# Kernel optimization log

Hardware: AMD Instinct MI355X
Metric: run time of the kernel (lower is better)

Reference implementation:

```python
import jax, jax.numpy as jnp
import numpy as np

B, S, D = 1, 2048, 2048
NH, NKV, HD = 32, 8, 64
EPS = 1e-5
SCALE = float(HD) ** 0.5


def _rope(x, cos, sin):
    # x: [b, h, s, hd]; cos/sin: [s, hd//2]; interleaved-pair rotary (executorch style)
    xr = x[..., 0::2]
    xi = x[..., 1::2]
    c = cos[None, None, :, :]
    s = sin[None, None, :, :]
    out_r = xr * c - xi * s
    out_i = xr * s + xi * c
    return jnp.stack([out_r, out_i], axis=-1).reshape(x.shape)


def _rmsnorm(x, w):
    var = jnp.mean(x * x, axis=-1, keepdims=True)
    return x * jax.lax.rsqrt(var + EPS) * w


def setup_inputs() -> dict:
    key = jax.random.key(0)
    ks = jax.random.split(key, 6)
    hidden_states = jax.random.normal(ks[0], (B, S, D), dtype=jnp.float32)
    # standard Llama rope tables, theta=10000
    inv_freq = 1.0 / (10000.0 ** (np.arange(0, HD, 2, dtype=np.float32) / HD))
    t = np.arange(S, dtype=np.float32)
    ang = np.outer(t, inv_freq)  # [S, HD//2]
    freqs_cos = jnp.asarray(np.cos(ang), dtype=jnp.float32)
    freqs_sin = jnp.asarray(np.sin(ang), dtype=jnp.float32)
    # additive causal mask [1,1,S,S]
    causal = jnp.tril(jnp.ones((S, S), dtype=bool))
    atten_mask = jnp.where(causal, 0.0, -1e9).astype(jnp.float32)[None, None]
    sd = 1.0 / np.sqrt(D)
    wq = jax.random.normal(ks[1], (NH * HD, D), dtype=jnp.float32) * sd
    wk = jax.random.normal(ks[2], (NKV * HD, D), dtype=jnp.float32) * sd
    wv = jax.random.normal(ks[3], (NKV * HD, D), dtype=jnp.float32) * sd
    wo = jax.random.normal(ks[4], (D, NH * HD), dtype=jnp.float32) * sd
    q_norm_w = jnp.ones((HD,), dtype=jnp.float32)
    k_norm_w = jnp.ones((HD,), dtype=jnp.float32)
    return dict(hidden_states=hidden_states, freqs_cos=freqs_cos, freqs_sin=freqs_sin,
                atten_mask=atten_mask, wq=wq, wk=wk, wv=wv, wo=wo,
                q_norm_w=q_norm_w, k_norm_w=k_norm_w)


def reference(hidden_states, freqs_cos, freqs_sin, atten_mask, wq, wk, wv, wo, q_norm_w, k_norm_w):
    b, s, _ = hidden_states.shape
    n_rep = NH // NKV
    # fused QKV projections (Linear: x @ W.T)
    q = (hidden_states @ wq.T).reshape(b, s, NH, HD).transpose(0, 2, 1, 3)   # [b,nh,s,hd]
    k = (hidden_states @ wk.T).reshape(b, s, NKV, HD).transpose(0, 2, 1, 3)  # [b,nkv,s,hd]
    v = (hidden_states @ wv.T).reshape(b, s, NKV, HD).transpose(0, 2, 1, 3)
    # RoPE, then QK RMSNorm (qk_norm_before_rope=False)
    q = _rope(q, freqs_cos, freqs_sin)
    k = _rope(k, freqs_cos, freqs_sin)
    q = _rmsnorm(q, q_norm_w)
    k = _rmsnorm(k, k_norm_w)
    # no KV cache (prefill): kh = k^T, vh = v, then GQA repeat
    kh = jnp.repeat(k, n_rep, axis=1)  # [b,nh,s,hd]
    vh = jnp.repeat(v, n_rep, axis=1)
    attn = jnp.einsum('bhqd,bhkd->bhqk', q, kh) / SCALE
    attn = jax.nn.softmax(attn + atten_mask, axis=-1)
    y = jnp.einsum('bhqk,bhkd->bhqd', attn, vh)
    y = y.transpose(0, 2, 1, 3).reshape(b, s, NH * HD)
    y = y @ wo.T
    # module returns (y, [kh], [vh]); kh stored transposed (b,nh,hd,s)
    return (y, kh.transpose(0, 1, 3, 2), vh)
```

## Files before the change

kernel.cpp:

```cpp
#include <hip/hip_runtime.h>
#include <cstdint>
#include <cstddef>

#define S_   2048
#define D_   2048
#define NH_  32
#define NKV_ 8
#define HD_  64

using bf16x8 = __attribute__((ext_vector_type(8))) __bf16;
using f32x4  = __attribute__((ext_vector_type(4))) float;

#define AS_GLOBAL(p) (const __attribute__((address_space(1))) void*)(p)
#define AS_LDS(p)    (__attribute__((address_space(3))) void*)(p)

__device__ __forceinline__ float b2f(uint u) {
  union { uint u; float f; } c; c.u = u << 16; return c.f;
}

__global__ __launch_bounds__(256) void cvt_all(
    const float* __restrict__ hs, const float* __restrict__ wq,
    const float* __restrict__ wk, const float* __restrict__ wv,
    const float* __restrict__ wo,
    __bf16* __restrict__ hs_bf, __bf16* __restrict__ wq_bf,
    __bf16* __restrict__ wk_bf, __bf16* __restrict__ wv_bf,
    __bf16* __restrict__ wo_bf) {
  int i = blockIdx.x * 256 + threadIdx.x;
  const float* src; __bf16* dst; int base;
  if (i < 1048576)      { src = hs; dst = hs_bf; base = 0; }
  else if (i < 2097152) { src = wq; dst = wq_bf; base = 1048576; }
  else if (i < 2359296) { src = wk; dst = wk_bf; base = 2097152; }
  else if (i < 2621440) { src = wv; dst = wv_bf; base = 2359296; }
  else                  { src = wo; dst = wo_bf; base = 2621440; }
  i -= base;
  const float4 v = reinterpret_cast<const float4*>(src)[i];
  __bf16 t[4] = {(__bf16)v.x, (__bf16)v.y, (__bf16)v.z, (__bf16)v.w};
  reinterpret_cast<uint2*>(dst)[i] = *reinterpret_cast<uint2*>(t);
}

__device__ __forceinline__ void gemm_compute_step(
    const char* ldsA, const char* ldsB, f32x4 (&acc)[4][4],
    int l15, int lg, int wm, int wn) {
  bf16x8 af[4][2], bfr[4][2];
#pragma unroll
  for (int f = 0; f < 4; ++f) {
    const int arow = wm*64 + f*16 + l15;
    const int brow = wn*64 + f*16 + l15;
#pragma unroll
    for (int ks = 0; ks < 2; ++ks) {
      af[f][ks] = *reinterpret_cast<const bf16x8*>(
          ldsA + arow*128 + (((ks*4 + lg) ^ (arow & 7)) << 4));
      bfr[f][ks] = *reinterpret_cast<const bf16x8*>(
          ldsB + brow*128 + (((ks*4 + lg) ^ (brow & 7)) << 4));
    }
  }
#pragma unroll
  for (int mf = 0; mf < 4; ++mf)
#pragma unroll
    for (int nf = 0; nf < 4; ++nf) {
      acc[mf][nf] = __builtin_amdgcn_mfma_f32_16x16x32_bf16(
          af[mf][0], bfr[nf][0], acc[mf][nf], 0, 0, 0);
      acc[mf][nf] = __builtin_amdgcn_mfma_f32_16x16x32_bf16(
          af[mf][1], bfr[nf][1], acc[mf][nf], 0, 0, 0);
    }
}

template <int MODE>
__device__ __forceinline__ void gemm_tile_128_bf(
    char (*lds)[32768],
    const __bf16* __restrict__ A, const __bf16* __restrict__ B,
    __bf16* __restrict__ C, int K, int N, int m0, int n0,
    const float* __restrict__ cosT, const float* __restrict__ sinT,
    const float* __restrict__ nw) {
  const int tid = threadIdx.x;
  const int l = tid & 63;
  const int w = tid >> 6;
  const int l15 = l & 15, lg = l >> 4;
  const int wm = w >> 1, wn = w & 1;

  f32x4 acc[4][4] = {};

  const int srow   = tid >> 3;
  const int schunk = (tid & 7) ^ (srow & 7);
  const __bf16* gA = A + (size_t)(m0 + srow) * K + schunk * 8;
  const __bf16* gB = B + (size_t)(n0 + srow) * K + schunk * 8;
  const int ldst = tid * 16;
  const int nt = K >> 6;

#pragma unroll
  for (int i = 0; i < 4; ++i) {
    __builtin_amdgcn_global_load_lds(AS_GLOBAL(gA + (size_t)i*32*K),
                                     AS_LDS(&lds[0][i*4096 + ldst]), 16, 0, 0);
    __builtin_amdgcn_global_load_lds(AS_GLOBAL(gB + (size_t)i*32*K),
                                     AS_LDS(&lds[0][16384 + i*4096 + ldst]), 16, 0, 0);
  }
  __syncthreads();

  int cur = 0;
  for (int t = 0; t < nt; ++t) {
    if (t + 1 < nt) {
      const int k0 = (t + 1) * 64;
      char* dA = &lds[cur ^ 1][0];
      char* dB = &lds[cur ^ 1][16384];
#pragma unroll
      for (int i = 0; i < 4; ++i) {
        __builtin_amdgcn_global_load_lds(AS_GLOBAL(gA + (size_t)i*32*K + k0),
                                         AS_LDS(dA + i*4096 + ldst), 16, 0, 0);
        __builtin_amdgcn_global_load_lds(AS_GLOBAL(gB + (size_t)i*32*K + k0),
                                         AS_LDS(dB + i*4096 + ldst), 16, 0, 0);
      }
    }
    gemm_compute_step(&lds[cur][0], &lds[cur][16384], acc, l15, lg, wm, wn);
    __syncthreads();
    cur ^= 1;
  }

  if constexpr (MODE == 0) {
#pragma unroll
    for (int mf = 0; mf < 4; ++mf)
#pragma unroll
      for (int nf = 0; nf < 4; ++nf)
#pragma unroll
        for (int r = 0; r < 4; ++r)
          C[(size_t)(m0 + wm*64 + mf*16 + lg*4 + r) * N + n0 + wn*64 + nf*16 + l15]
              = (__bf16)acc[mf][nf][r];
  } else {
    const float fin = (MODE == 1) ? 0.180336880111120426f : 1.0f;
    float wv_[4];
#pragma unroll
    for (int nf = 0; nf < 4; ++nf) wv_[nf] = nw[nf*16 + l15];
    const int odd = l15 & 1;
#pragma unroll
    for (int mf = 0; mf < 4; ++mf) {
#pragma unroll
      for (int r = 0; r < 4; ++r) {
        const int row = m0 + wm*64 + mf*16 + lg*4 + r;
        float ro[4];
        float ssq = 0.f;
#pragma unroll
        for (int nf = 0; nf < 4; ++nf) {
          const float v = acc[mf][nf][r];
          const float p = __shfl_xor(v, 1);
          const int d2 = (nf*16 + l15) >> 1;
          const float c  = cosT[row*32 + d2];
          const float sn = sinT[row*32 + d2];
          ro[nf] = odd ? fmaf(p, sn, v*c) : fmaf(v, c, -p*sn);
          ssq = fmaf(ro[nf], ro[nf], ssq);
        }
        ssq += __shfl_xor(ssq, 1);
        ssq += __shfl_xor(ssq, 2);
        ssq += __shfl_xor(ssq, 4);
        ssq += __shfl_xor(ssq, 8);
        const float rinv = rsqrtf(ssq * (1.0f/64.0f) + 1e-5f);
#pragma unroll
        for (int nf = 0; nf < 4; ++nf)
          C[(size_t)row * N + n0 + wn*64 + nf*16 + l15]
              = (__bf16)(ro[nf] * rinv * wv_[nf] * fin);
      }
    }
  }
}

__device__ __forceinline__ void gemm_tile_128_d2(
    const __bf16* __restrict__ A, const __bf16* __restrict__ B,
    float* __restrict__ C, int K, int N, int m0, int n0) {
  __shared__ __align__(16) char lds[3][32768];
  const int tid = threadIdx.x;
  const int l = tid & 63;
  const int w = tid >> 6;
  const int l15 = l & 15, lg = l >> 4;
  const int wm = w >> 1, wn = w & 1;

  f32x4 acc[4][4] = {};

  const int srow   = tid >> 3;
  const int schunk = (tid & 7) ^ (srow & 7);
  const __bf16* gA = A + (size_t)(m0 + srow) * K + schunk * 8;
  const __bf16* gB = B + (size_t)(n0 + srow) * K + schunk * 8;
  const int ldst = tid * 16;
  const int nt = K >> 6;

#pragma unroll
  for (int i = 0; i < 4; ++i) {
    __builtin_amdgcn_global_load_lds(AS_GLOBAL(gA + (size_t)i*32*K),
                                     AS_LDS(&lds[0][i*4096 + ldst]), 16, 0, 0);
    __builtin_amdgcn_global_load_lds(AS_GLOBAL(gB + (size_t)i*32*K),
                                     AS_LDS(&lds[0][16384 + i*4096 + ldst]), 16, 0, 0);
  }
#pragma unroll
  for (int i = 0; i < 4; ++i) {
    __builtin_amdgcn_global_load_lds(AS_GLOBAL(gA + (size_t)i*32*K + 64),
                                     AS_LDS(&lds[1][i*4096 + ldst]), 16, 0, 0);
    __builtin_amdgcn_global_load_lds(AS_GLOBAL(gB + (size_t)i*32*K + 64),
                                     AS_LDS(&lds[1][16384 + i*4096 + ldst]), 16, 0, 0);
  }

  char* p0 = &lds[0][0];
  char* p1 = &lds[1][0];
  char* p2 = &lds[2][0];

  for (int t = 0; t < nt; ++t) {
    if (t + 1 < nt) asm volatile("s_waitcnt vmcnt(8)" ::: "memory");
    else            asm volatile("s_waitcnt vmcnt(0)" ::: "memory");
    __builtin_amdgcn_s_barrier();

    if (t + 2 < nt) {
      const int k0 = (t + 2) * 64;
#pragma unroll
      for (int i = 0; i < 4; ++i) {
        __builtin_amdgcn_global_load_lds(AS_GLOBAL(gA + (size_t)i*32*K + k0),
                                         AS_LDS(p2 + i*4096 + ldst), 16, 0, 0);
        __builtin_amdgcn_global_load_lds(AS_GLOBAL(gB + (size_t)i*32*K + k0),
                                         AS_LDS(p2 + 16384 + i*4096 + ldst), 16, 0, 0);
      }
    }

    gemm_compute_step(p0, p0 + 16384, acc, l15, lg, wm, wn);

    char* tmp = p0; p0 = p1; p1 = p2; p2 = tmp;
  }

#pragma unroll
  for (int mf = 0; mf < 4; ++mf)
#pragma unroll
    for (int nf = 0; nf < 4; ++nf)
#pragma unroll
      for (int r = 0; r < 4; ++r)
        C[(size_t)(m0 + wm*64 + mf*16 + lg*4 + r) * N + n0 + wn*64 + nf*16 + l15]
            = acc[mf][nf][r];
}

__global__ __launch_bounds__(256) void gemm_qkv(
    const __bf16* __restrict__ hs,
    const __bf16* __restrict__ wq, const __bf16* __restrict__ wk,
    const __bf16* __restrict__ wv,
    __bf16* __restrict__ qbf, __bf16* __restrict__ kbf, __bf16* __restrict__ vp,
    const float* __restrict__ fcos, const float* __restrict__ fsin,
    const float* __restrict__ qw, const float* __restrict__ kw) {
  __shared__ __align__(16) char lds[2][32768];
  const int bx = blockIdx.x;
  const int m0 = blockIdx.y * 128;
  if (bx < 16) {
    gemm_tile_128_bf<1>(lds, hs, wq, qbf, 2048, 2048, m0, bx*128, fcos, fsin, qw);
  } else if (bx < 20) {
    gemm_tile_128_bf<2>(lds, hs, wk, kbf, 2048, 512, m0, (bx-16)*128, fcos, fsin, kw);
  } else {
    gemm_tile_128_bf<0>(lds, hs, wv, vp, 2048, 512, m0, (bx-20)*128,
                        nullptr, nullptr, nullptr);
  }
}

__global__ __launch_bounds__(256) void gemm_wo(
    const __bf16* __restrict__ ypre, const __bf16* __restrict__ wo,
    float* __restrict__ y) {
  gemm_tile_128_d2(ypre, wo, y, 2048, 2048, blockIdx.y * 128, blockIdx.x * 128);
}

__global__ __launch_bounds__(256) void transpose_kv(
    const __bf16* __restrict__ kpost, float* __restrict__ khT,
    const __bf16* __restrict__ vp, float* __restrict__ vh,
    __bf16* __restrict__ vtbf) {
  __shared__ float tl[64][68];
  const int kvh = blockIdx.y;
  const int t = threadIdx.x;
  if (blockIdx.x < 32) {
    const int s0 = blockIdx.x * 64;
    {
      const int d0 = (t & 15) * 4;
      const int sl = t >> 4;
#pragma unroll
      for (int rep = 0; rep < 4; ++rep) {
        const int srow = sl + rep*16;
        const uint2 v = *reinterpret_cast<const uint2*>(
            &kpost[(size_t)(s0 + srow)*(NKV_*HD_) + kvh*HD_ + d0]);
        tl[d0+0][srow] = b2f(v.x & 0xffff);
        tl[d0+1][srow] = b2f(v.x >> 16);
        tl[d0+2][srow] = b2f(v.y & 0xffff);
        tl[d0+3][srow] = b2f(v.y >> 16);
      }
    }
    __syncthreads();
    {
      const int d  = t >> 2;
      const int s4 = (t & 3) * 16;
#pragma unroll
      for (int c = 0; c < 4; ++c) {
        float4 v;
        v.x = tl[d][s4+c*4+0]; v.y = tl[d][s4+c*4+1];
        v.z = tl[d][s4+c*4+2]; v.w = tl[d][s4+c*4+3];
#pragma unroll
        for (int r = 0; r < 4; ++r) {
          *reinterpret_cast<float4*>(
              &khT[((size_t)(kvh*4 + r)*HD_ + d)*S_ + s0 + s4 + c*4]) = v;
        }
      }
    }
  } else {
    const int s0 = (blockIdx.x - 32) * 64;
    const int srow = t >> 2, dc = (t & 3) * 16;
    const __bf16* src = &vp[(size_t)(s0 + srow)*(NKV_*HD_) + kvh*HD_ + dc];
    const uint4 a = reinterpret_cast<const uint4*>(src)[0];
    const uint4 b = reinterpret_cast<const uint4*>(src)[1];
    float f[16];
    f[0]=b2f(a.x&0xffff); f[1]=b2f(a.x>>16); f[2]=b2f(a.y&0xffff); f[3]=b2f(a.y>>16);
    f[4]=b2f(a.z&0xffff); f[5]=b2f(a.z>>16); f[6]=b2f(a.w&0xffff); f[7]=b2f(a.w>>16);
    f[8]=b2f(b.x&0xffff); f[9]=b2f(b.x>>16); f[10]=b2f(b.y&0xffff); f[11]=b2f(b.y>>16);
    f[12]=b2f(b.z&0xffff); f[13]=b2f(b.z>>16); f[14]=b2f(b.w&0xffff); f[15]=b2f(b.w>>16);
#pragma unroll
    for (int i = 0; i < 16; ++i) tl[srow][dc + i] = f[i];
#pragma unroll
    for (int r = 0; r < 4; ++r) {
      float* dst = &vh[((size_t)(kvh*4 + r)*S_ + s0 + srow)*HD_ + dc];
#pragma unroll
      for (int cc = 0; cc < 4; ++cc) {
        float4 v4 = {f[cc*4+0], f[cc*4+1], f[cc*4+2], f[cc*4+3]};
        reinterpret_cast<float4*>(dst)[cc] = v4;
      }
    }
    __syncthreads();
    const int dr = t >> 2, sc = (t & 3) * 16;
    __bf16 vals[16];
#pragma unroll
    for (int i = 0; i < 16; ++i) vals[i] = (__bf16)tl[sc + i][dr];
    uint4* dst = reinterpret_cast<uint4*>(&vtbf[((size_t)(kvh*64 + dr))*S_ + s0 + sc]);
    dst[0] = reinterpret_cast<uint4*>(vals)[0];
    dst[1] = reinterpret_cast<uint4*>(vals)[1];
  }
}

__device__ __forceinline__ uint pack2bf(float a, float b) {
  __bf16 x = (__bf16)a, y = (__bf16)b;
  const uint ux = (uint)*reinterpret_cast<ushort*>(&x);
  const uint uy = (uint)*reinterpret_cast<ushort*>(&y);
  return ux | (uy << 16);
}

__device__ __forceinline__ void qk_tile_T(
    const char* kldh, bf16x8 qf0, bf16x8 qf1, f32x4 (&s_)[4],
    int l15, int lg) {
  __builtin_amdgcn_s_setprio(1);
#pragma unroll
  for (int nb = 0; nb < 4; ++nb) {
    const int row = nb*16 + l15;
    const int bc  = lg*16;
    const bf16x8 kb0 = *reinterpret_cast<const bf16x8*>(
        kldh + row*128 + ((bc)      ^ ((row & 7) << 4)));
    const bf16x8 kb1 = *reinterpret_cast<const bf16x8*>(
        kldh + row*128 + ((bc + 64) ^ ((row & 7) << 4)));
    f32x4 t = f32x4{0.f, 0.f, 0.f, 0.f};
    t = __builtin_amdgcn_mfma_f32_16x16x32_bf16(kb0, qf0, t, 0, 0, 0);
    t = __builtin_amdgcn_mfma_f32_16x16x32_bf16(kb1, qf1, t, 0, 0, 0);
    s_[nb] = t;
  }
  __builtin_amdgcn_s_setprio(0);
}

__device__ __forceinline__ void softmax_pv_T(
    f32x4 (&s_)[4], float& m_, float& l_, f32x4 (&o_)[4],
    char* pldw, const char* vbase, int l15, int lg) {
  float mx = fmaxf(fmaxf(s_[0][0], s_[0][1]), fmaxf(s_[0][2], s_[0][3]));
#pragma unroll
  for (int nb = 1; nb < 4; ++nb) {
    mx = fmaxf(mx, fmaxf(fmaxf(s_[nb][0], s_[nb][1]),
                         fmaxf(s_[nb][2], s_[nb][3])));
  }
  mx = fmaxf(mx, __shfl_xor(mx, 16));
  mx = fmaxf(mx, __shfl_xor(mx, 32));

  if (!__all(mx <= m_ + 8.f)) {
    const float mnew = fmaxf(m_, mx);
    const float scl = exp2f(m_ - mnew);
    m_ = mnew;
    l_ *= scl;
#pragma unroll
    for (int nb = 0; nb < 4; ++nb) {
      o_[nb][0] *= scl; o_[nb][1] *= scl; o_[nb][2] *= scl; o_[nb][3] *= scl;
    }
  }

  const int swz = (l15 & 7) << 4;
  float ls = 0.f;
#pragma unroll
  for (int nb = 0; nb < 4; ++nb) {
    float p0 = exp2f(s_[nb][0] - m_);
    float p1 = exp2f(s_[nb][1] - m_);
    float p2 = exp2f(s_[nb][2] - m_);
    float p3 = exp2f(s_[nb][3] - m_);
    ls += (p0 + p1) + (p2 + p3);
    *reinterpret_cast<uint*>(pldw + ((l15*128 + nb*32 + lg*8)     ^ swz)) = pack2bf(p0, p1);
    *reinterpret_cast<uint*>(pldw + ((l15*128 + nb*32 + lg*8 + 4) ^ swz)) = pack2bf(p2, p3);
  }
  ls += __shfl_xor(ls, 16);
  ls += __shfl_xor(ls, 32);
  l_ += ls;

  const bf16x8 pb0 = *reinterpret_cast<const bf16x8*>(
      pldw + ((l15*128 + lg*16)      ^ swz));
  const bf16x8 pb1 = *reinterpret_cast<const bf16x8*>(
      pldw + ((l15*128 + lg*16 + 64) ^ swz));

  __builtin_amdgcn_s_setprio(1);
#pragma unroll
  for (int nb = 0; nb < 4; ++nb) {
    const int row = nb*16 + l15;
    const int bc  = lg*16;
    const bf16x8 v0 = *reinterpret_cast<const bf16x8*>(
        vbase + row*128 + ((bc)      ^ ((row & 7) << 4)));
    const bf16x8 v1 = *reinterpret_cast<const bf16x8*>(
        vbase + row*128 + ((bc + 64) ^ ((row & 7) << 4)));
    f32x4 t = o_[nb];
    t = __builtin_amdgcn_mfma_f32_16x16x32_bf16(v0, pb0, t, 0, 0, 0);
    t = __builtin_amdgcn_mfma_f32_16x16x32_bf16(v1, pb1, t, 0, 0, 0);
    o_[nb] = t;
  }
  __builtin_amdgcn_s_setprio(0);
}

__device__ __forceinline__ void mask_diag_T(f32x4 (&s_)[4], int l15, int lg, int wg) {
  const int qrow = wg*16 + l15;
#pragma unroll
  for (int nb = 0; nb < 4; ++nb)
#pragma unroll
    for (int r = 0; r < 4; ++r)
      if (nb*16 + lg*4 + r > qrow) s_[nb][r] = -1e30f;
}

__global__ __launch_bounds__(512, 4) void flash_attn_mfma(
    const __bf16* __restrict__ qbf, const __bf16* __restrict__ kbf,
    const __bf16* __restrict__ vtbf, __bf16* __restrict__ ypre) {
  __shared__ __align__(16) char smem[49152];

  const int h   = blockIdx.y;
  const int pi  = blockIdx.x;
  const int qbA = pi, qbB = 31 - pi;
  const int SS  = (qbB >> 1) + 1;
  const int kvh = h >> 2;
  const int tid = threadIdx.x;
  const int l   = tid & 63;
  const int w   = tid >> 6;
  const int g   = tid >> 8;
  const int wg  = w & 3;
  const int l15 = l & 15;
  const int lg  = l >> 4;

  char* kldg = smem + g*8192;
  char* vtlg = smem + 16384 + g*8192;
  char* pldw = smem + 32768 + w*2048;

  const int ts = tid & 255;
  const int j  = ts >> 2;
  const int c0 = (ts & 3) * 16;
  const int b0 = (j*128 + c0*2)      ^ ((j & 7) << 4);
  const int b1 = (j*128 + c0*2 + 16) ^ ((j & 7) << 4);
  const __bf16* ksrc = kbf  + (size_t)(g*64 + j)*(NKV_*HD_) + kvh*HD_ + c0;
  const __bf16* vsrc = vtbf + (size_t)(kvh*64 + j)*S_ + g*64 + c0;

  bf16x8 qfA0, qfA1, qfB0, qfB1;
  {
    const __bf16* qa = qbf + (size_t)(qbA*64 + wg*16 + l15)*D_ + h*HD_ + lg*8;
    qfA0 = *reinterpret_cast<const bf16x8*>(qa);
    qfA1 = *reinterpret_cast<const bf16x8*>(qa + 32);
    const __bf16* qb = qbf + (size_t)(qbB*64 + wg*16 + l15)*D_ + h*HD_ + lg*8;
    qfB0 = *reinterpret_cast<const bf16x8*>(qb);
    qfB1 = *reinterpret_cast<const bf16x8*>(qb + 32);
  }

  f32x4 oA[4], oB[4];
#pragma unroll
  for (int nb = 0; nb < 4; ++nb) {
    oA[nb] = f32x4{0.f, 0.f, 0.f, 0.f};
    oB[nb] = f32x4{0.f, 0.f, 0.f, 0.f};
  }
  float mA = -1e30f, lA = 0.f, mB = -1e30f, lB = 0.f;

  uint4 kr0 = reinterpret_cast<const uint4*>(ksrc)[0];
  uint4 kr1 = reinterpret_cast<const uint4*>(ksrc + 8)[0];
  uint4 vr0 = reinterpret_cast<const uint4*>(vsrc)[0];
  uint4 vr1 = reinterpret_cast<const uint4*>(vsrc + 8)[0];

  for (int st = 0; st < SS; ++st) {
    __syncthreads();
    *reinterpret_cast<uint4*>(kldg + b0) = kr0;
    *reinterpret_cast<uint4*>(kldg + b1) = kr1;
    *reinterpret_cast<uint4*>(vtlg + b0) = vr0;
    *reinterpret_cast<uint4*>(vtlg + b1) = vr1;
    __syncthreads();

    if (st + 1 < SS) {
      const __bf16* kn = ksrc + (size_t)(st + 1)*128*(NKV_*HD_);
      const __bf16* vn = vsrc + (size_t)(st + 1)*128;
      kr0 = reinterpret_cast<const uint4*>(kn)[0];
      kr1 = reinterpret_cast<const uint4*>(kn + 8)[0];
      vr0 = reinterpret_cast<const uint4*>(vn)[0];
      vr1 = reinterpret_cast<const uint4*>(vn + 8)[0];
    }

    const int kt = 2*st + g;
    if (kt <= qbB) {
      f32x4 s_[4];
      qk_tile_T(kldg, qfB0, qfB1, s_, l15, lg);
      if (kt == qbB) mask_diag_T(s_, l15, lg, wg);
      softmax_pv_T(s_, mB, lB, oB, pldw, vtlg, l15, lg);
    }
    if (kt <= qbA) {
      f32x4 s_[4];
      qk_tile_T(kldg, qfA0, qfA1, s_, l15, lg);
      if (kt == qbA) mask_diag_T(s_, l15, lg, wg);
      softmax_pv_T(s_, mA, lA, oA, pldw, vtlg, l15, lg);
    }
  }

  float* ox = reinterpret_cast<float*>(smem);
  float* ml = reinterpret_cast<float*>(smem + 20480);
  float* po = ox + (wg*64 + l)*17;
  float* pm = ml + (wg*64 + l)*9;

  __syncthreads();
  if (g == 1) {
#pragma unroll
    for (int nb = 0; nb < 4; ++nb)
#pragma unroll
      for (int r = 0; r < 4; ++r) po[nb*4 + r] = oB[nb][r];
    pm[0] = mB; pm[1] = lB;
  }
  __syncthreads();
  if (g == 0) {
    const float m1 = pm[0], l1 = pm[1];
    const float m = fmaxf(mB, m1);
    const float s0 = exp2f(mB - m), s1 = exp2f(m1 - m);
    lB = lB*s0 + l1*s1;
#pragma unroll
    for (int nb = 0; nb < 4; ++nb)
#pragma unroll
      for (int r = 0; r < 4; ++r)
        oB[nb][r] = oB[nb][r]*s0 + po[nb*4 + r]*s1;
  }
  __syncthreads();
  if (g == 1) {
#pragma unroll
    for (int nb = 0; nb < 4; ++nb)
#pragma unroll
      for (int r = 0; r < 4; ++r) po[nb*4 + r] = oA[nb][r];
    pm[0] = mA; pm[1] = lA;
  }
  __syncthreads();
  if (g == 0) {
    const float m1 = pm[0], l1 = pm[1];
    const float m = fmaxf(mA, m1);
    const float s0 = exp2f(mA - m), s1 = exp2f(m1 - m);
    lA = lA*s0 + l1*s1;
#pragma unroll
    for (int nb = 0; nb < 4; ++nb)
#pragma unroll
      for (int r = 0; r < 4; ++r)
        oA[nb][r] = oA[nb][r]*s0 + po[nb*4 + r]*s1;

    const float rlA = 1.0f / lA, rlB = 1.0f / lB;
    const size_t rowA = (size_t)(qbA*64 + wg*16 + l15)*D_ + h*HD_;
    const size_t rowB = (size_t)(qbB*64 + wg*16 + l15)*D_ + h*HD_;
#pragma unroll
    for (int nb = 0; nb < 4; ++nb) {
      uint2 pa, pb;
      pa.x = pack2bf(oA[nb][0]*rlA, oA[nb][1]*rlA);
      pa.y = pack2bf(oA[nb][2]*rlA, oA[nb][3]*rlA);
      pb.x = pack2bf(oB[nb][0]*rlB, oB[nb][1]*rlB);
      pb.y = pack2bf(oB[nb][2]*rlB, oB[nb][3]*rlB);
      *reinterpret_cast<uint2*>(&ypre[rowA + nb*16 + lg*4]) = pa;
      *reinterpret_cast<uint2*>(&ypre[rowB + nb*16 + lg*4]) = pb;
    }
  }
}

extern "C" void kernel_launch(void* const* d_in, const int* in_sizes, int n_in,
                              void* d_out, int out_size, void* d_ws, size_t ws_size,
                              hipStream_t stream) {
  (void)in_sizes; (void)n_in; (void)out_size;
  const float* hs   = (const float*)d_in[0];
  const float* fcos = (const float*)d_in[1];
  const float* fsin = (const float*)d_in[2];
  const float* wq = (const float*)d_in[4];
  const float* wk = (const float*)d_in[5];
  const float* wv = (const float*)d_in[6];
  const float* wo = (const float*)d_in[7];
  const float* qw = (const float*)d_in[8];
  const float* kw = (const float*)d_in[9];

  float* out = (float*)d_out;
  float* y   = out;
  float* khT = out + 4194304;
  float* vh  = out + 8388608;

  __bf16* qbf   = (__bf16*)y;
  __bf16* kbf   = (__bf16*)((char*)y + 8*1024*1024);
  __bf16* vtbf  = (__bf16*)((char*)y + 10*1024*1024);
  __bf16* hs_bf = (__bf16*)khT;
  __bf16* wq_bf = (__bf16*)((char*)khT + 8*1024*1024);
  __bf16* wk_bf = (__bf16*)vh;
  __bf16* wv_bf = (__bf16*)((char*)vh + 2*1024*1024);

  const size_t need = (size_t)40 * 1024 * 1024;
  if (ws_size < need) return;
  char* ws = (char*)d_ws;
  __bf16* vp_bf   = (__bf16*)(ws);
  __bf16* ypre_bf = (__bf16*)(ws + 2*1024*1024);
  __bf16* wo_bf   = (__bf16*)(ws + 10*1024*1024);

  cvt_all<<<14336, 256, 0, stream>>>(hs, wq, wk, wv, wo,
                                     hs_bf, wq_bf, wk_bf, wv_bf, wo_bf);

  gemm_qkv<<<dim3(24, 16), 256, 0, stream>>>(hs_bf, wq_bf, wk_bf, wv_bf,
                                             qbf, kbf, vp_bf,
                                             fcos, fsin, qw, kw);

  transpose_kv<<<dim3(64, 8), 256, 0, stream>>>(kbf, khT, vp_bf, vh, vtbf);

  flash_attn_mfma<<<dim3(16, 32), 512, 0, stream>>>(qbf, kbf, vtbf, ypre_bf);

  gemm_wo<<<dim3(16, 16), 256, 0, stream>>>(ypre_bf, wo_bf, y);
}
```

Measured before the change: 139.6 us.

## Triple-buffer QKV GEMM and widen Q tiles to 128x256

Reworks the fused QKV projection GEMM into a three-stage LDS pipeline that uses explicit vmcnt waits and a single barrier per k-step, instead of double buffering with two syncs. Q-projection blocks now compute 128x256 tiles (8 N-fragments per wave), so the A tile is reused across more columns and the grid shrinks from 24 to 16 columns. The RoPE+RMSNorm epilogue is regrouped per 64-wide head. The cost is 144KB of LDS per block, which limits occupancy to one block per CU, plus more accumulator registers for the wide tiles.

```diff
diff --git a/kernel.cpp b/kernel.cpp
--- a/kernel.cpp
+++ b/kernel.cpp
@@ -65,9 +65,9 @@
     }
 }
 
-template <int MODE>
-__device__ __forceinline__ void gemm_tile_128_bf(
-    char (*lds)[32768],
+template <int MODE, int NW>
+__device__ __forceinline__ void gemm_tile_d2x(
+    char (*lds)[49152],
     const __bf16* __restrict__ A, const __bf16* __restrict__ B,
     __bf16* __restrict__ C, int K, int N, int m0, int n0,
     const float* __restrict__ cosT, const float* __restrict__ sinT,
@@ -78,7 +78,7 @@
   const int l15 = l & 15, lg = l >> 4;
   const int wm = w >> 1, wn = w & 1;
 
-  f32x4 acc[4][4] = {};
+  f32x4 acc[4][NW] = {};
 
   const int srow   = tid >> 3;
   const int schunk = (tid & 7) ^ (srow & 7);
@@ -87,75 +87,109 @@
   const int ldst = tid * 16;
   const int nt = K >> 6;
 
-#pragma unroll
-  for (int i = 0; i < 4; ++i) {
-    __builtin_amdgcn_global_load_lds(AS_GLOBAL(gA + (size_t)i*32*K),
-                                     AS_LDS(&lds[0][i*4096 + ldst]), 16, 0, 0);
-    __builtin_amdgcn_global_load_lds(AS_GLOBAL(gB + (size_t)i*32*K),
-                                     AS_LDS(&lds[0][16384 + i*4096 + ldst]), 16, 0, 0);
-  }
-  __syncthreads();
-
-  int cur = 0;
+  auto stage = [&](char* buf, int k0) {
+#pragma unroll
+    for (int i = 0; i < 4; ++i)
+      __builtin_amdgcn_global_load_lds(AS_GLOBAL(gA + (size_t)i*32*K + k0),
+                                       AS_LDS(buf + i*4096 + ldst), 16, 0, 0);
+#pragma unroll
+    for (int i = 0; i < NW; ++i)
+      __builtin_amdgcn_global_load_lds(AS_GLOBAL(gB + (size_t)i*32*K + k0),
+                                       AS_LDS(buf + 16384 + i*4096 + ldst), 16, 0, 0);
+  };
+
+  stage(&lds[0][0], 0);
+  stage(&lds[1][0], 64);
+
+  char* p0 = &lds[0][0];
+  char* p1 = &lds[1][0];
+  char* p2 = &lds[2][0];
+
   for (int t = 0; t < nt; ++t) {
     if (t + 1 < nt) {
-      const int k0 = (t + 1) * 64;
-      char* dA = &lds[cur ^ 1][0];
-      char* dB = &lds[cur ^ 1][16384];
-#pragma unroll
-      for (int i = 0; i < 4; ++i) {
-        __builtin_amdgcn_global_load_lds(AS_GLOBAL(gA + (size_t)i*32*K + k0),
-                                         AS_LDS(dA + i*4096 + ldst), 16, 0, 0);
-        __builtin_amdgcn_global_load_lds(AS_GLOBAL(gB + (size_t)i*32*K + k0),
-                                         AS_LDS(dB + i*4096 + ldst), 16, 0, 0);
+      if constexpr (NW == 8) asm volatile("s_waitcnt vmcnt(12)" ::: "memory");
+      else                   asm volatile("s_waitcnt vmcnt(8)"  ::: "memory");
+    } else {
+      asm volatile("s_waitcnt vmcnt(0)" ::: "memory");
+    }
+    __builtin_amdgcn_s_barrier();
+
+    if (t + 2 < nt) stage(p2, (t + 2) * 64);
+
+    {
+      bf16x8 af[4][2];
+#pragma unroll
+      for (int f = 0; f < 4; ++f) {
+        const int arow = wm*64 + f*16 + l15;
+#pragma unroll
+        for (int ks = 0; ks < 2; ++ks)
+          af[f][ks] = *reinterpret_cast<const bf16x8*>(
+              p0 + arow*128 + (((ks*4 + lg) ^ (arow & 7)) << 4));
       }
-    }
-    gemm_compute_step(&lds[cur][0], &lds[cur][16384], acc, l15, lg, wm, wn);
-    __syncthreads();
-    cur ^= 1;
+#pragma unroll
+      for (int nf = 0; nf < NW; ++nf) {
+        const int brow = wn*(NW*16) + nf*16 + l15;
+        const bf16x8 b0 = *reinterpret_cast<const bf16x8*>(
+            p0 + 16384 + brow*128 + (((lg)     ^ (brow & 7)) << 4));
+        const bf16x8 b1 = *reinterpret_cast<const bf16x8*>(
+            p0 + 16384 + brow*128 + (((4 + lg) ^ (brow & 7)) << 4));
+#pragma unroll
+        for (int mf = 0; mf < 4; ++mf) {
+          acc[mf][nf] = __builtin_amdgcn_mfma_f32_16x16x32_bf16(
+              af[mf][0], b0, acc[mf][nf], 0, 0, 0);
+          acc[mf][nf] = __builtin_amdgcn_mfma_f32_16x16x32_bf16(
+              af[mf][1], b1, acc[mf][nf], 0, 0, 0);
+        }
+      }
+    }
+
+    char* tmp = p0; p0 = p1; p1 = p2; p2 = tmp;
   }
 
   if constexpr (MODE == 0) {
 #pragma unroll
     for (int mf = 0; mf < 4; ++mf)
 #pragma unroll
-      for (int nf = 0; nf < 4; ++nf)
+      for (int nf = 0; nf < NW; ++nf)
 #pragma unroll
         for (int r = 0; r < 4; ++r)
-          C[(size_t)(m0 + wm*64 + mf*16 + lg*4 + r) * N + n0 + wn*64 + nf*16 + l15]
-              = (__bf16)acc[mf][nf][r];
+          C[(size_t)(m0 + wm*64 + mf*16 + lg*4 + r) * N
+            + n0 + wn*(NW*16) + nf*16 + l15] = (__bf16)acc[mf][nf][r];
   } else {
     const float fin = (MODE == 1) ? 0.180336880111120426f : 1.0f;
-    float wv_[4];
-#pragma unroll
-    for (int nf = 0; nf < 4; ++nf) wv_[nf] = nw[nf*16 + l15];
+    float wv4[4];
+#pragma unroll
+    for (int j = 0; j < 4; ++j) wv4[j] = nw[j*16 + l15];
     const int odd = l15 & 1;
 #pragma unroll
     for (int mf = 0; mf < 4; ++mf) {
 #pragma unroll
       for (int r = 0; r < 4; ++r) {
         const int row = m0 + wm*64 + mf*16 + lg*4 + r;
-        float ro[4];
-        float ssq = 0.f;
-#pragma unroll
-        for (int nf = 0; nf < 4; ++nf) {
-          const float v = acc[mf][nf][r];
-          const float p = __shfl_xor(v, 1);
-          const int d2 = (nf*16 + l15) >> 1;
-          const float c  = cosT[row*32 + d2];
-          const float sn = sinT[row*32 + d2];
-          ro[nf] = odd ? fmaf(p, sn, v*c) : fmaf(v, c, -p*sn);
-          ssq = fmaf(ro[nf], ro[nf], ssq);
+#pragma unroll
+        for (int grp = 0; grp < NW/4; ++grp) {
+          float ro[4];
+          float ssq = 0.f;
+#pragma unroll
+          for (int j = 0; j < 4; ++j) {
+            const float v = acc[mf][grp*4 + j][r];
+            const float p = __shfl_xor(v, 1);
+            const int d2 = (j*16 + l15) >> 1;
+            const float c  = cosT[row*32 + d2];
+            const float sn = sinT[row*32 + d2];
+            ro[j] = odd ? fmaf(p, sn, v*c) : fmaf(v, c, -p*sn);
+            ssq = fmaf(ro[j], ro[j], ssq);
+          }
+          ssq += __shfl_xor(ssq, 1);
+          ssq += __shfl_xor(ssq, 2);
+          ssq += __shfl_xor(ssq, 4);
+          ssq += __shfl_xor(ssq, 8);
+          const float rinv = rsqrtf(ssq * (1.0f/64.0f) + 1e-5f);
+#pragma unroll
+          for (int j = 0; j < 4; ++j)
+            C[(size_t)row * N + n0 + wn*(NW*16) + (grp*4 + j)*16 + l15]
+                = (__bf16)(ro[j] * rinv * wv4[j] * fin);
         }
-        ssq += __shfl_xor(ssq, 1);
-        ssq += __shfl_xor(ssq, 2);
-        ssq += __shfl_xor(ssq, 4);
-        ssq += __shfl_xor(ssq, 8);
-        const float rinv = rsqrtf(ssq * (1.0f/64.0f) + 1e-5f);
-#pragma unroll
-        for (int nf = 0; nf < 4; ++nf)
-          C[(size_t)row * N + n0 + wn*64 + nf*16 + l15]
-              = (__bf16)(ro[nf] * rinv * wv_[nf] * fin);
       }
     }
   }
@@ -237,15 +271,17 @@
     __bf16* __restrict__ qbf, __bf16* __restrict__ kbf, __bf16* __restrict__ vp,
     const float* __restrict__ fcos, const float* __restrict__ fsin,
     const float* __restrict__ qw, const float* __restrict__ kw) {
-  __shared__ __align__(16) char lds[2][32768];
+  __shared__ __align__(16) char lds[3][49152];
   const int bx = blockIdx.x;
   const int m0 = blockIdx.y * 128;
-  if (bx < 16) {
-    gemm_tile_128_bf<1>(lds, hs, wq, qbf, 2048, 2048, m0, bx*128, fcos, fsin, qw);
-  } else if (bx < 20) {
-    gemm_tile_128_bf<2>(lds, hs, wk, kbf, 2048, 512, m0, (bx-16)*128, fcos, fsin, kw);
+  if (bx < 8) {
+    gemm_tile_d2x<1, 8>(lds, hs, wq, qbf, 2048, 2048, m0, bx*256,
+                        fcos, fsin, qw);
+  } else if (bx < 12) {
+    gemm_tile_d2x<2, 4>(lds, hs, wk, kbf, 2048, 512, m0, (bx-8)*128,
+                        fcos, fsin, kw);
   } else {
-    gemm_tile_128_bf<0>(lds, hs, wv, vp, 2048, 512, m0, (bx-20)*128,
+    gemm_tile_d2x<0, 4>(lds, hs, wv, vp, 2048, 512, m0, (bx-12)*128,
                         nullptr, nullptr, nullptr);
   }
 }
@@ -608,7 +644,7 @@
   cvt_all<<<14336, 256, 0, stream>>>(hs, wq, wk, wv, wo,
                                      hs_bf, wq_bf, wk_bf, wv_bf, wo_bf);
 
-  gemm_qkv<<<dim3(24, 16), 256, 0, stream>>>(hs_bf, wq_bf, wk_bf, wv_bf,
+  gemm_qkv<<<dim3(16, 16), 256, 0, stream>>>(hs_bf, wq_bf, wk_bf, wv_bf,
                                              qbf, kbf, vp_bf,
                                              fcos, fsin, qw, kw);
 
```

Measured after the change: 149.8 us. +7.3%, slower.
